# Kernel optimization log

Hardware: AMD Instinct MI355X
Metric: run time of the kernel (lower is better)

Reference implementation:

```python
import jax, jax.numpy as jnp
import numpy as np


def setup_inputs() -> dict:
    key = jax.random.key(0)
    ks = jax.random.split(key, 7)
    B, N, K, D = 256, 50, 12, 128
    return {
        "batch_size": B,
        "itm_emb": jax.random.normal(ks[0], (B, N, D), jnp.float32),
        "ave_sess_itms_emb": jax.random.normal(ks[1], (B, N, D), jnp.float32),
        "glob_adj_itm_embs": jax.random.normal(ks[2], (B, N, K, D), jnp.float32),
        "glob_adj_wgt_embs": jax.random.normal(ks[3], (B, N, K), jnp.float32),
        "w1": jax.random.normal(ks[4], (D + 1, D), jnp.float32) * 0.1,
        "w2": jax.random.normal(ks[5], (D, 1), jnp.float32) * 0.1,
        "w3": jax.random.normal(ks[6], (2 * D, D), jnp.float32) * 0.1,
    }


def reference(batch_size, itm_emb, ave_sess_itms_emb, glob_adj_itm_embs,
              glob_adj_wgt_embs, w1, w2, w3):
    D = itm_emb.shape[-1]
    # [B,N,1,D] * [B,N,K,D] -> [B,N,K,D]; concat weight -> [B,N,K,D+1]
    alpha = ave_sess_itms_emb[:, :, None, :] * glob_adj_itm_embs
    alpha = jnp.concatenate([alpha, glob_adj_wgt_embs[..., None]], axis=-1)
    alpha = jnp.einsum('bnkc,cd->bnkd', alpha, w1)          # [B,N,K,D]
    alpha = jax.nn.leaky_relu(alpha, negative_slope=0.2)
    alpha = jnp.einsum('bnkd,do->bnk', alpha, w2)           # [B,N,K]
    alpha = jax.nn.softmax(alpha, axis=-1)[..., None]       # [B,N,K,1]
    att = jnp.sum(alpha * glob_adj_itm_embs, axis=-2)       # [B,N,D]
    g = jnp.concatenate([itm_emb, att], axis=-1)            # [B,N,2D]
    # dropout with p=0.0 / eval mode is identity
    g = jnp.einsum('bnc,cd->bnd', g, w3)
    g = g.reshape(batch_size, -1, D)
    return jax.nn.relu(g)
```

## Files before the change

### kernel.cpp

```cpp
#include <hip/hip_runtime.h>

#define DD 128
#define KADJ 12
#define BN_TOTAL 12800

typedef float f32x4 __attribute__((ext_vector_type(4)));
typedef float f32x2 __attribute__((ext_vector_type(2)));
typedef __bf16 bf16x8 __attribute__((ext_vector_type(8)));
typedef __bf16 bf16x4 __attribute__((ext_vector_type(4)));
typedef unsigned int u32;

__device__ __forceinline__ bf16x8 cvt8(f32x4 a, f32x4 b) {
    bf16x8 r;
    r[0] = (__bf16)a[0]; r[1] = (__bf16)a[1]; r[2] = (__bf16)a[2]; r[3] = (__bf16)a[3];
    r[4] = (__bf16)b[0]; r[5] = (__bf16)b[1]; r[6] = (__bf16)b[2]; r[7] = (__bf16)b[3];
    return r;
}

__device__ __forceinline__ bf16x8 mul8(bf16x8 a, bf16x8 b) {
    bf16x8 r;
    #pragma unroll
    for (int i = 0; i < 8; ++i) r[i] = (__bf16)((float)a[i] * (float)b[i]);
    return r;
}

__global__ void k_prep(const float* __restrict__ w1, const float* __restrict__ w3,
                       __bf16* __restrict__ w1f, __bf16* __restrict__ w3f) {
    int idx = blockIdx.x * 256 + threadIdx.x;
    int lane = (idx >> 3) & 63, e = idx & 7;
    int l = lane & 15, gg = lane >> 4;
    if (idx < 16384) {
        int fi = idx >> 9, n = fi >> 2, ks = fi & 3;
        int k = ks * 32 + gg * 8 + e;
        w1f[idx] = (__bf16)w1[k * DD + n * 16 + l];
    } else {
        int j = idx - 16384;
        int fi = j >> 9, n = fi >> 3, ks = fi & 7;
        int k = ks * 32 + gg * 8 + e;
        w3f[j] = (__bf16)w3[k * DD + n * 16 + l];
    }
}

__launch_bounds__(256)
__global__ void k_att(const float* __restrict__ ave, const float* __restrict__ adj,
                      const float* __restrict__ wgt, const float* __restrict__ w1,
                      const float* __restrict__ w2, const __bf16* __restrict__ w1f,
                      float* __restrict__ att_out) {
    __shared__ unsigned char lds[54528];
    const int t = threadIdx.x;
    const int lane = t & 63;
    const int w = t >> 6;
    const int l = lane & 15, g = lane >> 4;
    const int bn0 = blockIdx.x * 16 + w * 4;
    const size_t R = (size_t)bn0 * KADJ;

    unsigned char* adjb = lds + w * 12288;
    unsigned char* aveb = lds + 49152 + w * 1088;
    float* sco = (float*)(lds + 53504 + w * 256);

    {
        const float* src = adj + R * DD;
        const int r = lane >> 5;
        const int c4 = (lane & 31) * 4;
        const int u = c4 >> 3, bo = (c4 & 7) * 2;
        #pragma unroll
        for (int i = 0; i < 24; ++i) {
            int row = i * 2 + r;
            f32x4 v = __builtin_nontemporal_load(
                reinterpret_cast<const f32x4*>(src + (size_t)row * DD + c4));
            bf16x4 bv;
            bv[0] = (__bf16)v[0]; bv[1] = (__bf16)v[1];
            bv[2] = (__bf16)v[2]; bv[3] = (__bf16)v[3];
            *reinterpret_cast<bf16x4*>(adjb + row * 256 + ((u ^ (row & 15)) << 4) + bo) = bv;
        }
    }
    {
        const int a = lane >> 4;
        const int c8 = (lane & 15) * 8;
        const float* src = ave + (size_t)(bn0 + a) * DD + c8;
        f32x4 v0 = *reinterpret_cast<const f32x4*>(src);
        f32x4 v1 = *reinterpret_cast<const f32x4*>(src + 4);
        *reinterpret_cast<bf16x8*>(aveb + a * 272 + c8 * 2) = cvt8(v0, v1);
    }

    float w1r[8], w2v[8];
    #pragma unroll
    for (int n = 0; n < 8; ++n) {
        w1r[n] = w1[128 * DD + n * 16 + l];
        w2v[n] = w2[n * 16 + l];
    }

    #pragma unroll
    for (int rt = 0; rt < 3; ++rt) {
        const int lr = rt * 16 + l;
        const int arow = lr >= 36 ? 3 : lr >= 24 ? 2 : lr >= 12 ? 1 : 0;
        f32x4 acc[8];
        #pragma unroll
        for (int n = 0; n < 8; ++n) acc[n] = f32x4{0.f, 0.f, 0.f, 0.f};
        #pragma unroll
        for (int ks = 0; ks < 4; ++ks) {
            bf16x8 adjf = *reinterpret_cast<const bf16x8*>(
                adjb + lr * 256 + (((ks * 4 + g) ^ (lr & 15)) << 4));
            bf16x8 avef = *reinterpret_cast<const bf16x8*>(
                aveb + arow * 272 + ks * 64 + g * 16);
            bf16x8 af = mul8(adjf, avef);
            const __bf16* bp = w1f + ((size_t)ks * 64 + lane) * 8;
            #pragma unroll
            for (int n = 0; n < 8; ++n) {
                bf16x8 bfr = *reinterpret_cast<const bf16x8*>(bp + (size_t)n * 2048);
                acc[n] = __builtin_amdgcn_mfma_f32_16x16x32_bf16(af, bfr, acc[n], 0, 0, 0);
            }
        }
        float wv[4];
        #pragma unroll
        for (int j = 0; j < 4; ++j)
            wv[j] = wgt[R + rt * 16 + g * 4 + j];
        float p[4] = {0.f, 0.f, 0.f, 0.f};
        #pragma unroll
        for (int n = 0; n < 8; ++n) {
            #pragma unroll
            for (int j = 0; j < 4; ++j) {
                float h = fmaf(wv[j], w1r[n], acc[n][j]);
                h = h > 0.f ? h : 0.2f * h;
                p[j] = fmaf(h, w2v[n], p[j]);
            }
        }
        #pragma unroll
        for (int j = 0; j < 4; ++j) {
            p[j] += __shfl_xor(p[j], 1, 64);
            p[j] += __shfl_xor(p[j], 2, 64);
            p[j] += __shfl_xor(p[j], 4, 64);
            p[j] += __shfl_xor(p[j], 8, 64);
        }
        if (l == 0)
            *reinterpret_cast<f32x4*>(&sco[rt * 16 + g * 4]) = f32x4{p[0], p[1], p[2], p[3]};
    }

    #pragma unroll
    for (int b = 0; b < 4; ++b) {
        float s[KADJ];
        float mx = -1e30f;
        #pragma unroll
        for (int k = 0; k < KADJ; ++k) { s[k] = sco[b * 12 + k]; mx = fmaxf(mx, s[k]); }
        float sum = 0.f;
        #pragma unroll
        for (int k = 0; k < KADJ; ++k) { s[k] = __expf(s[k] - mx); sum += s[k]; }
        float inv = 1.f / sum;
        float a0 = 0.f, a1 = 0.f;
        #pragma unroll
        for (int k = 0; k < KADJ; ++k) {
            int row = b * 12 + k;
            u32 pk = *reinterpret_cast<const u32*>(
                adjb + row * 256 + ((((lane >> 2) ^ (row & 15))) << 4) + (lane & 3) * 4);
            float alpha = s[k] * inv;
            float e0 = __builtin_bit_cast(float, pk << 16);
            float e1 = __builtin_bit_cast(float, pk & 0xFFFF0000u);
            a0 = fmaf(alpha, e0, a0);
            a1 = fmaf(alpha, e1, a1);
        }
        *reinterpret_cast<f32x2*>(att_out + (size_t)(bn0 + b) * DD + lane * 2) = f32x2{a0, a1};
    }
}

__launch_bounds__(64)
__global__ void k_out(const float* __restrict__ itm, const float* att,
                      const __bf16* __restrict__ w3f, float* outp) {
    const int lane = threadIdx.x & 63;
    const int l = lane & 15, g = lane >> 4;
    const int R0 = blockIdx.x * 16;
    const int row = R0 + l;

    bf16x8 afr[8];
    const float* ip = itm + (size_t)row * DD;
    #pragma unroll
    for (int s = 0; s < 4; ++s) {
        int c = s * 32 + g * 8;
        f32x4 a0 = *reinterpret_cast<const f32x4*>(ip + c);
        f32x4 a1 = *reinterpret_cast<const f32x4*>(ip + c + 4);
        afr[s] = cvt8(a0, a1);
    }
    const float* ap = att + (size_t)row * DD;
    #pragma unroll
    for (int s = 0; s < 4; ++s) {
        int c = s * 32 + g * 8;
        f32x4 a0 = *reinterpret_cast<const f32x4*>(ap + c);
        f32x4 a1 = *reinterpret_cast<const f32x4*>(ap + c + 4);
        afr[4 + s] = cvt8(a0, a1);
    }

    f32x4 acc[8];
    #pragma unroll
    for (int n = 0; n < 8; ++n) acc[n] = f32x4{0.f, 0.f, 0.f, 0.f};
    #pragma unroll
    for (int s = 0; s < 8; ++s) {
        const __bf16* bp = w3f + ((size_t)s * 64 + lane) * 8;
        #pragma unroll
        for (int n = 0; n < 8; ++n) {
            bf16x8 bfr = *reinterpret_cast<const bf16x8*>(bp + (size_t)n * 4096);
            acc[n] = __builtin_amdgcn_mfma_f32_16x16x32_bf16(afr[s], bfr, acc[n], 0, 0, 0);
        }
    }

    #pragma unroll
    for (int n = 0; n < 8; ++n) {
        #pragma unroll
        for (int j = 0; j < 4; ++j)
            outp[(size_t)(R0 + g * 4 + j) * DD + n * 16 + l] = fmaxf(acc[n][j], 0.f);
    }
}

extern "C" void kernel_launch(void* const* d_in, const int* in_sizes, int n_in,
                              void* d_out, int out_size, void* d_ws, size_t ws_size,
                              hipStream_t stream) {
    const float* itm = (const float*)d_in[1];
    const float* ave = (const float*)d_in[2];
    const float* adj = (const float*)d_in[3];
    const float* wgt = (const float*)d_in[4];
    const float* w1  = (const float*)d_in[5];
    const float* w2  = (const float*)d_in[6];
    const float* w3  = (const float*)d_in[7];
    float* outp = (float*)d_out;

    __bf16* w1f = (__bf16*)d_ws;
    __bf16* w3f = (__bf16*)((char*)d_ws + 32 * 1024);

    k_prep<<<dim3(192), dim3(256), 0, stream>>>(w1, w3, w1f, w3f);
    k_att<<<dim3(BN_TOTAL / 16), dim3(256), 0, stream>>>(ave, adj, wgt, w1, w2, w1f, outp);
    k_out<<<dim3(BN_TOTAL / 16), dim3(64), 0, stream>>>(itm, outp, w3f, outp);
}
```

Before: 48.21 us.

## Remap attention kernel to one wave per item, stage w1 in LDS

Restructures k_att so each wave handles a single (b,n) item with its 12 neighbor rows in one 16-row MFMA tile, and 512-thread blocks cover 8 items. The block's first step copies the pre-swizzled bf16 w1 fragments into LDS for reuse instead of each wave reading them from global memory, and the softmax is now done entirely with cross-lane shuffles instead of an LDS score buffer. k_out is also widened to 4 waves per block. The trade-off is that 4 of the 16 MFMA rows are padding (25% wasted matrix work), plus an extra block-wide barrier and a 32 KB weight copy per block.

```diff
diff --git a/kernel.cpp b/kernel.cpp
--- a/kernel.cpp
+++ b/kernel.cpp
@@ -7,7 +7,7 @@
 typedef float f32x4 __attribute__((ext_vector_type(4)));
 typedef float f32x2 __attribute__((ext_vector_type(2)));
 typedef __bf16 bf16x8 __attribute__((ext_vector_type(8)));
-typedef __bf16 bf16x4 __attribute__((ext_vector_type(4)));
+typedef __bf16 bf16x2 __attribute__((ext_vector_type(2)));
 typedef unsigned int u32;
 
 __device__ __forceinline__ bf16x8 cvt8(f32x4 a, f32x4 b) {
@@ -41,47 +41,43 @@
     }
 }
 
-__launch_bounds__(256)
+__launch_bounds__(512, 4)
 __global__ void k_att(const float* __restrict__ ave, const float* __restrict__ adj,
                       const float* __restrict__ wgt, const float* __restrict__ w1,
                       const float* __restrict__ w2, const __bf16* __restrict__ w1f,
                       float* __restrict__ att_out) {
-    __shared__ unsigned char lds[54528];
+    __shared__ unsigned char lds[32768 + 8 * (3072 + 272)];
     const int t = threadIdx.x;
     const int lane = t & 63;
     const int w = t >> 6;
     const int l = lane & 15, g = lane >> 4;
-    const int bn0 = blockIdx.x * 16 + w * 4;
-    const size_t R = (size_t)bn0 * KADJ;
-
-    unsigned char* adjb = lds + w * 12288;
-    unsigned char* aveb = lds + 49152 + w * 1088;
-    float* sco = (float*)(lds + 53504 + w * 256);
+    const int bn = blockIdx.x * 8 + w;
+    const size_t abase = (size_t)bn * (KADJ * DD);
+
+    __bf16* w1s = (__bf16*)lds;
+    unsigned char* adjb = lds + 32768 + w * 3072;
+    unsigned char* aveb = lds + 32768 + 8 * 3072 + w * 272;
 
     {
-        const float* src = adj + R * DD;
-        const int r = lane >> 5;
-        const int c4 = (lane & 31) * 4;
-        const int u = c4 >> 3, bo = (c4 & 7) * 2;
-        #pragma unroll
-        for (int i = 0; i < 24; ++i) {
-            int row = i * 2 + r;
-            f32x4 v = __builtin_nontemporal_load(
-                reinterpret_cast<const f32x4*>(src + (size_t)row * DD + c4));
-            bf16x4 bv;
-            bv[0] = (__bf16)v[0]; bv[1] = (__bf16)v[1];
-            bv[2] = (__bf16)v[2]; bv[3] = (__bf16)v[3];
-            *reinterpret_cast<bf16x4*>(adjb + row * 256 + ((u ^ (row & 15)) << 4) + bo) = bv;
-        }
+        const f32x4* src = (const f32x4*)w1f;
+        f32x4* dst = (f32x4*)w1s;
+        #pragma unroll
+        for (int p = 0; p < 4; ++p) dst[p * 512 + t] = src[p * 512 + t];
+    }
+    #pragma unroll
+    for (int i = 0; i < 3; ++i) {
+        int row = i * 4 + g;
+        const float* gs = adj + abase + (size_t)row * DD + l * 8;
+        f32x4 v0 = __builtin_nontemporal_load(reinterpret_cast<const f32x4*>(gs));
+        f32x4 v1 = __builtin_nontemporal_load(reinterpret_cast<const f32x4*>(gs + 4));
+        *reinterpret_cast<bf16x8*>(adjb + row * 256 + ((l ^ row) << 4)) = cvt8(v0, v1);
     }
     {
-        const int a = lane >> 4;
-        const int c8 = (lane & 15) * 8;
-        const float* src = ave + (size_t)(bn0 + a) * DD + c8;
-        f32x4 v0 = *reinterpret_cast<const f32x4*>(src);
-        f32x4 v1 = *reinterpret_cast<const f32x4*>(src + 4);
-        *reinterpret_cast<bf16x8*>(aveb + a * 272 + c8 * 2) = cvt8(v0, v1);
-    }
+        f32x2 v = *reinterpret_cast<const f32x2*>(ave + (size_t)bn * DD + lane * 2);
+        bf16x2 bv; bv[0] = (__bf16)v[0]; bv[1] = (__bf16)v[1];
+        *reinterpret_cast<bf16x2*>(aveb + lane * 4) = bv;
+    }
+    __syncthreads();
 
     float w1r[8], w2v[8];
     #pragma unroll
@@ -90,84 +86,92 @@
         w2v[n] = w2[n * 16 + l];
     }
 
-    #pragma unroll
-    for (int rt = 0; rt < 3; ++rt) {
-        const int lr = rt * 16 + l;
-        const int arow = lr >= 36 ? 3 : lr >= 24 ? 2 : lr >= 12 ? 1 : 0;
-        f32x4 acc[8];
-        #pragma unroll
-        for (int n = 0; n < 8; ++n) acc[n] = f32x4{0.f, 0.f, 0.f, 0.f};
-        #pragma unroll
-        for (int ks = 0; ks < 4; ++ks) {
-            bf16x8 adjf = *reinterpret_cast<const bf16x8*>(
-                adjb + lr * 256 + (((ks * 4 + g) ^ (lr & 15)) << 4));
-            bf16x8 avef = *reinterpret_cast<const bf16x8*>(
-                aveb + arow * 272 + ks * 64 + g * 16);
-            bf16x8 af = mul8(adjf, avef);
-            const __bf16* bp = w1f + ((size_t)ks * 64 + lane) * 8;
-            #pragma unroll
-            for (int n = 0; n < 8; ++n) {
-                bf16x8 bfr = *reinterpret_cast<const bf16x8*>(bp + (size_t)n * 2048);
-                acc[n] = __builtin_amdgcn_mfma_f32_16x16x32_bf16(af, bfr, acc[n], 0, 0, 0);
-            }
+    const int l2 = l < KADJ ? l : KADJ - 1;
+    f32x4 acc[8];
+    #pragma unroll
+    for (int n = 0; n < 8; ++n) acc[n] = f32x4{0.f, 0.f, 0.f, 0.f};
+    #pragma unroll
+    for (int ks = 0; ks < 4; ++ks) {
+        bf16x8 adjf = *reinterpret_cast<const bf16x8*>(
+            adjb + l2 * 256 + (((ks * 4 + g) ^ l2) << 4));
+        bf16x8 avef = *reinterpret_cast<const bf16x8*>(aveb + ks * 64 + g * 16);
+        bf16x8 af = mul8(adjf, avef);
+        const __bf16* bp = w1s + ((size_t)ks * 64 + lane) * 8;
+        #pragma unroll
+        for (int n = 0; n < 8; ++n) {
+            bf16x8 bfr = *reinterpret_cast<const bf16x8*>(bp + (size_t)n * 2048);
+            acc[n] = __builtin_amdgcn_mfma_f32_16x16x32_bf16(af, bfr, acc[n], 0, 0, 0);
         }
-        float wv[4];
-        #pragma unroll
-        for (int j = 0; j < 4; ++j)
-            wv[j] = wgt[R + rt * 16 + g * 4 + j];
-        float p[4] = {0.f, 0.f, 0.f, 0.f};
-        #pragma unroll
-        for (int n = 0; n < 8; ++n) {
-            #pragma unroll
-            for (int j = 0; j < 4; ++j) {
-                float h = fmaf(wv[j], w1r[n], acc[n][j]);
-                h = h > 0.f ? h : 0.2f * h;
-                p[j] = fmaf(h, w2v[n], p[j]);
-            }
+    }
+
+    float wv[4];
+    #pragma unroll
+    for (int j = 0; j < 4; ++j) {
+        int r = g * 4 + j;
+        wv[j] = (r < KADJ) ? wgt[(size_t)bn * KADJ + r] : 0.f;
+    }
+    float p[4] = {0.f, 0.f, 0.f, 0.f};
+    #pragma unroll
+    for (int n = 0; n < 8; ++n) {
+        #pragma unroll
+        for (int j = 0; j < 4; ++j) {
+            float h = fmaf(wv[j], w1r[n], acc[n][j]);
+            h = h > 0.f ? h : 0.2f * h;
+            p[j] = fmaf(h, w2v[n], p[j]);
         }
-        #pragma unroll
-        for (int j = 0; j < 4; ++j) {
-            p[j] += __shfl_xor(p[j], 1, 64);
-            p[j] += __shfl_xor(p[j], 2, 64);
-            p[j] += __shfl_xor(p[j], 4, 64);
-            p[j] += __shfl_xor(p[j], 8, 64);
-        }
-        if (l == 0)
-            *reinterpret_cast<f32x4*>(&sco[rt * 16 + g * 4]) = f32x4{p[0], p[1], p[2], p[3]};
-    }
-
-    #pragma unroll
-    for (int b = 0; b < 4; ++b) {
-        float s[KADJ];
-        float mx = -1e30f;
-        #pragma unroll
-        for (int k = 0; k < KADJ; ++k) { s[k] = sco[b * 12 + k]; mx = fmaxf(mx, s[k]); }
-        float sum = 0.f;
-        #pragma unroll
-        for (int k = 0; k < KADJ; ++k) { s[k] = __expf(s[k] - mx); sum += s[k]; }
-        float inv = 1.f / sum;
-        float a0 = 0.f, a1 = 0.f;
-        #pragma unroll
-        for (int k = 0; k < KADJ; ++k) {
-            int row = b * 12 + k;
-            u32 pk = *reinterpret_cast<const u32*>(
-                adjb + row * 256 + ((((lane >> 2) ^ (row & 15))) << 4) + (lane & 3) * 4);
-            float alpha = s[k] * inv;
-            float e0 = __builtin_bit_cast(float, pk << 16);
-            float e1 = __builtin_bit_cast(float, pk & 0xFFFF0000u);
-            a0 = fmaf(alpha, e0, a0);
-            a1 = fmaf(alpha, e1, a1);
-        }
-        *reinterpret_cast<f32x2*>(att_out + (size_t)(bn0 + b) * DD + lane * 2) = f32x2{a0, a1};
-    }
-}
-
-__launch_bounds__(64)
+    }
+    #pragma unroll
+    for (int j = 0; j < 4; ++j) {
+        p[j] += __shfl_xor(p[j], 1, 64);
+        p[j] += __shfl_xor(p[j], 2, 64);
+        p[j] += __shfl_xor(p[j], 4, 64);
+        p[j] += __shfl_xor(p[j], 8, 64);
+        if (g == 3) p[j] = -1e30f;
+    }
+
+    float q0[4], q1[4], q2[4];
+    #pragma unroll
+    for (int j = 0; j < 4; ++j) {
+        q0[j] = __shfl_xor(p[j], 16, 64);
+        q1[j] = __shfl_xor(p[j], 32, 64);
+        q2[j] = __shfl_xor(q1[j], 16, 64);
+    }
+    float mx = -1e30f;
+    #pragma unroll
+    for (int j = 0; j < 4; ++j)
+        mx = fmaxf(mx, fmaxf(fmaxf(p[j], q0[j]), fmaxf(q1[j], q2[j])));
+    float ssum = 0.f;
+    #pragma unroll
+    for (int j = 0; j < 4; ++j) {
+        ssum += __expf(p[j] - mx);  ssum += __expf(q0[j] - mx);
+        ssum += __expf(q1[j] - mx); ssum += __expf(q2[j] - mx);
+    }
+    float inv = 1.f / ssum;
+
+    float a0 = 0.f, a1 = 0.f;
+    #pragma unroll
+    for (int k = 0; k < KADJ; ++k) {
+        int d = (k >> 2) ^ g, j = k & 3;
+        float sv = (d == 0) ? p[j] : (d == 1) ? q0[j] : (d == 2) ? q1[j] : q2[j];
+        float alpha = __expf(sv - mx) * inv;
+        u32 pk = *reinterpret_cast<const u32*>(
+            adjb + k * 256 + ((((lane >> 2) ^ k)) << 4) + (lane & 3) * 4);
+        float e0 = __builtin_bit_cast(float, pk << 16);
+        float e1 = __builtin_bit_cast(float, pk & 0xFFFF0000u);
+        a0 = fmaf(alpha, e0, a0);
+        a1 = fmaf(alpha, e1, a1);
+    }
+    *reinterpret_cast<f32x2*>(att_out + (size_t)bn * DD + lane * 2) = f32x2{a0, a1};
+}
+
+__launch_bounds__(256)
 __global__ void k_out(const float* __restrict__ itm, const float* att,
                       const __bf16* __restrict__ w3f, float* outp) {
-    const int lane = threadIdx.x & 63;
+    const int t = threadIdx.x;
+    const int lane = t & 63;
+    const int w = t >> 6;
     const int l = lane & 15, g = lane >> 4;
-    const int R0 = blockIdx.x * 16;
+    const int R0 = blockIdx.x * 64 + w * 16;
     const int row = R0 + l;
 
     bf16x8 afr[8];
@@ -225,6 +229,6 @@
     __bf16* w3f = (__bf16*)((char*)d_ws + 32 * 1024);
 
     k_prep<<<dim3(192), dim3(256), 0, stream>>>(w1, w3, w1f, w3f);
-    k_att<<<dim3(BN_TOTAL / 16), dim3(256), 0, stream>>>(ave, adj, wgt, w1, w2, w1f, outp);
-    k_out<<<dim3(BN_TOTAL / 16), dim3(64), 0, stream>>>(itm, outp, w3f, outp);
-}
+    k_att<<<dim3(BN_TOTAL / 8), dim3(512), 0, stream>>>(ave, adj, wgt, w1, w2, w1f, outp);
+    k_out<<<dim3(BN_TOTAL / 64), dim3(256), 0, stream>>>(itm, outp, w3f, outp);
+}
```

Measured after the change: 51.94 us. +7.7%, slower.
